# Kernel tuning notes

Measured on AMD Instinct MI355X. Metric: run time of the kernel, lower is better.

## Reference

```python
import jax, jax.numpy as jnp
import numpy as np

DIM = 512
HEADS = 8
DK = DIM // HEADS
MAX_LEN = 22118
EPS = 1e-5


def _layernorm(h, g, b):
    m = jnp.mean(h, axis=-1, keepdims=True)
    v = jnp.mean((h - m) ** 2, axis=-1, keepdims=True)
    return (h - m) / jnp.sqrt(v + EPS) * g + b


def setup_inputs() -> dict:
    key = jax.random.key(0)
    ks = jax.random.split(key, 16)
    B, S = 4, 2048
    xavier = lambda k, shp: jax.random.normal(k, shp, jnp.float32) * np.sqrt(2.0 / (shp[0] + shp[1]))
    return {
        "x": jax.random.normal(ks[0], (B, S, DIM), jnp.float32),
        "vis_data": jax.random.normal(ks[1], (B, S, DIM), jnp.float32),
        "coord1": jax.random.randint(ks[2], (B, S), 0, MAX_LEN, jnp.int32),
        "coord2": jax.random.randint(ks[3], (B, S), 0, MAX_LEN, jnp.int32),
        "emb1": jax.random.normal(ks[4], (MAX_LEN, DIM // 2), jnp.float32) * 0.02,
        "emb2": jax.random.normal(ks[5], (MAX_LEN, DIM // 2), jnp.float32) * 0.02,
        "wq": xavier(ks[6], (DIM, DIM)), "bq": jnp.zeros((DIM,), jnp.float32),
        "wk": xavier(ks[7], (DIM, DIM)), "bk": jnp.zeros((DIM,), jnp.float32),
        "wv": xavier(ks[8], (DIM, DIM)), "bv": jnp.zeros((DIM,), jnp.float32),
        "w1": xavier(ks[9], (DIM, DIM)), "b1": jnp.zeros((DIM,), jnp.float32),
        "g1": jnp.ones((DIM,), jnp.float32), "beta1": jnp.zeros((DIM,), jnp.float32),
        "w2": xavier(ks[10], (DIM, DIM)), "b2": jnp.zeros((DIM,), jnp.float32),
        "g2": jnp.ones((DIM,), jnp.float32), "beta2": jnp.zeros((DIM,), jnp.float32),
    }


def reference(x, vis_data, coord1, coord2, emb1, emb2, wq, bq, wk, bk, wv, bv,
              w1, b1, g1, beta1, w2, b2, g2, beta2):
    B, S, _ = x.shape
    # learned positional encoding: concat of two coordinate embeddings
    pos = jnp.concatenate([emb1[coord1], emb2[coord2]], axis=-1)  # [B,S,DIM]
    xp = x + pos
    # Q/K from vis_data, V from position-encoded x
    q = (vis_data @ wq + bq).reshape(B, S, HEADS, DK)
    k = (vis_data @ wk + bk).reshape(B, S, HEADS, DK)
    v = (xp @ wv + bv).reshape(B, S, HEADS, DK)
    scores = jnp.einsum("bqhd,bkhd->bhqk", q, k) / np.sqrt(DK).astype(np.float32)
    attn = jax.nn.softmax(scores, axis=-1)  # dropout is identity in eval
    out = jnp.einsum("bhqk,bkhd->bqhd", attn, v).reshape(B, S, DIM)
    # post-attention MLP stack (self.layer)
    h = jax.nn.leaky_relu(out @ w1 + b1, negative_slope=0.2)
    h = _layernorm(h, g1, beta1)
    h = jax.nn.leaky_relu(h @ w2 + b2, negative_slope=0.2)
    h = _layernorm(h, g2, beta2)
    return h
```

## Files before the change

### kernel.cpp

```cpp
#include <hip/hip_runtime.h>

#define DIM 512
#define SEQ 2048
#define MROWS 8192

typedef short short8 __attribute__((ext_vector_type(8)));
typedef float floatx4 __attribute__((ext_vector_type(4)));

__device__ __forceinline__ ushort f2bf(float f) {
  union { float f; unsigned u; } v; v.f = f;
  unsigned r = v.u + 0x7fff + ((v.u >> 16) & 1);
  return (ushort)(r >> 16);
}
__device__ __forceinline__ float bf2f(ushort u) {
  union { unsigned u; float f; } v; v.u = ((unsigned)u) << 16;
  return v.f;
}

__global__ __launch_bounds__(256) void prep_wtrans_kernel(
    const float* __restrict__ x, const float* __restrict__ vis,
    const int* __restrict__ c1, const int* __restrict__ c2,
    const float* __restrict__ e1, const float* __restrict__ e2,
    const float* __restrict__ wq, const float* __restrict__ wk,
    const float* __restrict__ wv, const float* __restrict__ w1,
    const float* __restrict__ w2,
    ushort* __restrict__ xp_bf, ushort* __restrict__ vis_bf,
    ushort* __restrict__ wt_qkv, ushort* __restrict__ wt1,
    ushort* __restrict__ wt2) {
  __shared__ float Ls[64 * 65];
  if (blockIdx.x < 4096) {
    int gid = blockIdx.x * 256 + threadIdx.x;
    int row = gid >> 7;
    int col = (gid & 127) * 4;
    float4 vv = *(const float4*)(vis + (size_t)row * 512 + col);
    ushort4 vb; vb.x = f2bf(vv.x); vb.y = f2bf(vv.y); vb.z = f2bf(vv.z); vb.w = f2bf(vv.w);
    *(ushort4*)(vis_bf + (size_t)row * 512 + col) = vb;
    float4 p;
    if (col < 256) p = *(const float4*)(e1 + (size_t)c1[row] * 256 + col);
    else           p = *(const float4*)(e2 + (size_t)c2[row] * 256 + col - 256);
    float4 xv = *(const float4*)(x + (size_t)row * 512 + col);
    ushort4 xb; xb.x = f2bf(xv.x + p.x); xb.y = f2bf(xv.y + p.y);
    xb.z = f2bf(xv.z + p.z); xb.w = f2bf(xv.w + p.w);
    *(ushort4*)(xp_bf + (size_t)row * 512 + col) = xb;
  } else {
    int bid = blockIdx.x - 4096;
    int mid = bid >> 6;
    int tile = bid & 63;
    int k0 = (tile >> 3) * 64, n0 = (tile & 7) * 64;
    const float* W = mid == 0 ? wq : mid == 1 ? wk : mid == 2 ? wv : mid == 3 ? w1 : w2;
    ushort* outp = mid < 3 ? (wt_qkv + (size_t)mid * 512 * 512) : (mid == 3 ? wt1 : wt2);
    float scale = (mid == 0) ? 0.125f : 1.0f;
    int r = threadIdx.x >> 4, c4 = (threadIdx.x & 15) * 4;
#pragma unroll
    for (int i = 0; i < 4; i++) {
      int row = i * 16 + r;
      float4 wv4 = *(const float4*)(W + (size_t)(k0 + row) * 512 + n0 + c4);
      Ls[row * 65 + c4 + 0] = wv4.x * scale;
      Ls[row * 65 + c4 + 1] = wv4.y * scale;
      Ls[row * 65 + c4 + 2] = wv4.z * scale;
      Ls[row * 65 + c4 + 3] = wv4.w * scale;
    }
    __syncthreads();
    int n = threadIdx.x >> 2, kc = (threadIdx.x & 3) * 16;
    ushort pk[16];
#pragma unroll
    for (int i = 0; i < 16; i++) pk[i] = f2bf(Ls[(kc + i) * 65 + n]);
    ushort* op = outp + (size_t)(n0 + n) * 512 + k0 + kc;
    *(uint4*)op = *(uint4*)pk;
    *(uint4*)(op + 8) = *(uint4*)(pk + 8);
  }
}

template <bool LEAKY>
__global__ __launch_bounds__(256, 4) void gemm_mfma(
    const ushort* __restrict__ A01, const ushort* __restrict__ A2,
    const ushort* __restrict__ Wt,
    const float* __restrict__ bias0, const float* __restrict__ bias1,
    const float* __restrict__ bias2,
    ushort* __restrict__ out0, ushort* __restrict__ out1,
    ushort* __restrict__ out2, float s0scale) {
  __shared__ __align__(16) ushort Sm[12288];
  ushort* As = Sm;
  ushort* Bs = Sm + 4096;
  int t = threadIdx.x;
  int seg = blockIdx.x >> 2;
  int nloc0 = (blockIdx.x & 3) * 128;
  int n0w = blockIdx.x * 128;
  int m0 = blockIdx.y * 64;
  const ushort* A = (seg < 2) ? A01 : A2;
  const float* bias = seg == 0 ? bias0 : seg == 1 ? bias1 : bias2;
  ushort* out = seg == 0 ? out0 : seg == 1 ? out1 : out2;
  float bscale = seg == 0 ? s0scale : 1.0f;

  int w = t >> 6, lane = t & 63;
  int wm = (w & 1) * 32, wn = (w >> 1) * 64;
  int quad = lane >> 4, lcol = lane & 15;
  int arow = t >> 2, ach = (t & 3) * 2;
  int brow = t >> 1, bch = (t & 1) * 4;

  floatx4 acc[2][4] = {};

  for (int k0 = 0; k0 < 512; k0 += 64) {
    __syncthreads();
#pragma unroll
    for (int i = 0; i < 2; i++) {
      int ch = ach + i;
      *(uint4*)(&As[arow * 64 + (ch ^ (arow & 7)) * 8]) =
          *(const uint4*)(A + (size_t)(m0 + arow) * 512 + k0 + ch * 8);
    }
#pragma unroll
    for (int j = 0; j < 4; j++) {
      int ch = bch + j;
      *(uint4*)(&Bs[brow * 64 + (ch ^ (brow & 7)) * 8]) =
          *(const uint4*)(Wt + (size_t)(n0w + brow) * 512 + k0 + ch * 8);
    }
    __syncthreads();
#pragma unroll
    for (int kc = 0; kc < 2; kc++) {
      int pch = ((kc * 4 + quad) ^ (lcol & 7)) * 8;
      short8 af[2], bfr[4];
#pragma unroll
      for (int i = 0; i < 2; i++)
        af[i] = *(const short8*)(&As[(wm + i * 16 + lcol) * 64 + pch]);
#pragma unroll
      for (int i = 0; i < 4; i++)
        bfr[i] = *(const short8*)(&Bs[(wn + i * 16 + lcol) * 64 + pch]);
#pragma unroll
      for (int mt = 0; mt < 2; mt++)
#pragma unroll
        for (int nt = 0; nt < 4; nt++)
          acc[mt][nt] = __builtin_amdgcn_mfma_f32_16x16x32_bf16(
              af[mt], bfr[nt], acc[mt][nt], 0, 0, 0);
    }
  }

  __syncthreads();
  float* Ls = (float*)Sm + w * 1088;
  int rr = lane >> 2, cc = (lane & 3) * 16;
#pragma unroll
  for (int mt = 0; mt < 2; mt++) {
#pragma unroll
    for (int nt = 0; nt < 4; nt++) {
      float bv = bias[nloc0 + wn + nt * 16 + lcol] * bscale;
#pragma unroll
      for (int r = 0; r < 4; r++) {
        float vv = acc[mt][nt][r] + bv;
        if (LEAKY) vv = vv >= 0.f ? vv : 0.2f * vv;
        Ls[(quad * 4 + r) * 68 + nt * 16 + lcol] = vv;
      }
    }
    asm volatile("s_waitcnt lgkmcnt(0)" ::: "memory");
    ushort pk[16];
#pragma unroll
    for (int i = 0; i < 16; i += 4) {
      float4 fv = *(const float4*)(&Ls[rr * 68 + cc + i]);
      pk[i] = f2bf(fv.x); pk[i + 1] = f2bf(fv.y);
      pk[i + 2] = f2bf(fv.z); pk[i + 3] = f2bf(fv.w);
    }
    ushort* op = out + (size_t)(m0 + wm + mt * 16 + rr) * 512 + nloc0 + wn + cc;
    *(uint4*)op = *(uint4*)pk;
    *(uint4*)(op + 8) = *(uint4*)(pk + 8);
    asm volatile("s_waitcnt lgkmcnt(0)" ::: "memory");
  }
}

__global__ __launch_bounds__(256, 2) void attn_mfma_kernel(
    const ushort* __restrict__ q, const ushort* __restrict__ k,
    const ushort* __restrict__ v, ushort* __restrict__ out) {
  __shared__ __align__(16) ushort Ks[128 * 64];
  __shared__ __align__(16) ushort Vt[64 * 128];
  __shared__ __align__(16) ushort Ps[4 * 32 * 64];
  int t = threadIdx.x;
  int blk = blockIdx.x;
  int qt = blk & 15, h = (blk >> 4) & 7, b = blk >> 7;
  int wave = t >> 6, lane = t & 63, quad = lane >> 4, lcol = lane & 15;
  int q0 = qt * 128 + wave * 32;
  const size_t base = (size_t)b * SEQ * 512 + h * 64;

  short8 qf[2][2];
#pragma unroll
  for (int qm = 0; qm < 2; qm++)
#pragma unroll
    for (int kc = 0; kc < 2; kc++)
      qf[qm][kc] = *(const short8*)(
          q + base + (size_t)(q0 + qm * 16 + lcol) * 512 + kc * 32 + quad * 8);

  floatx4 O[2][4] = {};
  float lsum[2][4] = {};

  ushort* Pw = Ps + wave * (32 * 64);
  int krow = t >> 1, khalf = t & 1;
  int pl = t & 63, dg = t >> 6;

  for (int kt = 0; kt < SEQ; kt += 128) {
    __syncthreads();
#pragma unroll
    for (int j = 0; j < 4; j++) {
      int ch = khalf * 4 + j;
      *(uint4*)(&Ks[krow * 64 + (ch ^ (krow & 7)) * 8]) =
          *(const uint4*)(k + base + (size_t)(kt + krow) * 512 + ch * 8);
    }
    {
      uint4 va[2], vb[2];
      const ushort* vr0 = v + base + (size_t)(kt + 2 * pl) * 512 + dg * 16;
      const ushort* vr1 = vr0 + 512;
      va[0] = *(const uint4*)(vr0); va[1] = *(const uint4*)(vr0 + 8);
      vb[0] = *(const uint4*)(vr1); vb[1] = *(const uint4*)(vr1 + 8);
      const ushort* a0 = (const ushort*)va;
      const ushort* a1 = (const ushort*)vb;
#pragma unroll
      for (int i = 0; i < 16; i++) {
        int dim = dg * 16 + i;
        unsigned pack = (unsigned)a0[i] | ((unsigned)a1[i] << 16);
        int pch = (pl >> 2) ^ (dim & 7);
        *(unsigned*)(&Vt[dim * 128 + pch * 8 + (pl & 3) * 2]) = pack;
      }
    }
    __syncthreads();

#pragma unroll
    for (int half = 0; half < 2; half++) {
#pragma unroll
      for (int qm = 0; qm < 2; qm++) {
        floatx4 S[4] = {};
#pragma unroll
        for (int kc = 0; kc < 2; kc++) {
          int pch = ((kc * 4 + quad) ^ (lcol & 7)) * 8;
#pragma unroll
          for (int jt4 = 0; jt4 < 4; jt4++) {
            int jrow = (half * 4 + jt4) * 16 + lcol;
            short8 kf = *(const short8*)(&Ks[jrow * 64 + pch]);
            S[jt4] = __builtin_amdgcn_mfma_f32_16x16x32_bf16(
                qf[qm][kc], kf, S[jt4], 0, 0, 0);
          }
        }
#pragma unroll
        for (int jt4 = 0; jt4 < 4; jt4++)
#pragma unroll
          for (int r = 0; r < 4; r++) {
            float p = __expf(S[jt4][r]);
            lsum[qm][r] += p;
            int prow = qm * 16 + quad * 4 + r;
            int pcol = jt4 * 16 + lcol;
            int pch2 = (pcol >> 3) ^ (prow & 7);
            Pw[prow * 64 + pch2 * 8 + (pcol & 7)] =
                (ushort)(__float_as_uint(p) >> 16);
          }
      }
      asm volatile("s_waitcnt lgkmcnt(0)" ::: "memory");
#pragma unroll
      for (int qm = 0; qm < 2; qm++) {
#pragma unroll
        for (int kc = 0; kc < 2; kc++) {
          short8 pf = *(const short8*)(
              &Pw[(qm * 16 + lcol) * 64 + ((kc * 4 + quad) ^ (lcol & 7)) * 8]);
#pragma unroll
          for (int nt = 0; nt < 4; nt++) {
            int dim = nt * 16 + lcol;
            int ch = half * 8 + kc * 4 + quad;
            short8 vf = *(const short8*)(&Vt[dim * 128 + (ch ^ (lcol & 7)) * 8]);
            O[qm][nt] = __builtin_amdgcn_mfma_f32_16x16x32_bf16(
                pf, vf, O[qm][nt], 0, 0, 0);
          }
        }
      }
    }
  }

#pragma unroll
  for (int qm = 0; qm < 2; qm++)
#pragma unroll
    for (int r = 0; r < 4; r++) {
#pragma unroll
      for (int m = 1; m <= 8; m <<= 1)
        lsum[qm][r] += __shfl_xor(lsum[qm][r], m, 64);
      lsum[qm][r] = 1.f / lsum[qm][r];
    }
#pragma unroll
  for (int qm = 0; qm < 2; qm++)
#pragma unroll
    for (int nt = 0; nt < 4; nt++)
#pragma unroll
      for (int r = 0; r < 4; r++)
        out[base + (size_t)(q0 + qm * 16 + quad * 4 + r) * 512 + nt * 16 + lcol] =
            f2bf(O[qm][nt][r] * lsum[qm][r]);
}

template <bool OUTF32>
__global__ __launch_bounds__(256) void ln_kernel(
    const ushort* __restrict__ h, const float* __restrict__ g,
    const float* __restrict__ beta, void* __restrict__ outv) {
  int wave = threadIdx.x >> 6, lane = threadIdx.x & 63;
  int row = blockIdx.x * 4 + wave;
  uint4 raw = *(const uint4*)(h + (size_t)row * 512 + lane * 8);
  const ushort* hu = (const ushort*)&raw;
  float vals[8];
#pragma unroll
  for (int i = 0; i < 8; i++) vals[i] = bf2f(hu[i]);
  float sum = 0.f;
#pragma unroll
  for (int i = 0; i < 8; i++) sum += vals[i];
#pragma unroll
  for (int off = 32; off >= 1; off >>= 1) sum += __shfl_xor(sum, off, 64);
  float mean = sum * (1.f / 512.f);
  float vs = 0.f;
#pragma unroll
  for (int i = 0; i < 8; i++) { float d = vals[i] - mean; vs += d * d; }
#pragma unroll
  for (int off = 32; off >= 1; off >>= 1) vs += __shfl_xor(vs, off, 64);
  float rstd = rsqrtf(vs * (1.f / 512.f) + 1e-5f);
  float4 gv0 = *(const float4*)(g + lane * 8);
  float4 gv1 = *(const float4*)(g + lane * 8 + 4);
  float4 bv0 = *(const float4*)(beta + lane * 8);
  float4 bv1 = *(const float4*)(beta + lane * 8 + 4);
  float gr[8] = {gv0.x, gv0.y, gv0.z, gv0.w, gv1.x, gv1.y, gv1.z, gv1.w};
  float br[8] = {bv0.x, bv0.y, bv0.z, bv0.w, bv1.x, bv1.y, bv1.z, bv1.w};
  float res[8];
#pragma unroll
  for (int i = 0; i < 8; i++) res[i] = (vals[i] - mean) * rstd * gr[i] + br[i];
  if (OUTF32) {
    float* op = (float*)outv + (size_t)row * 512 + lane * 8;
    float4 o0, o1;
    o0.x = res[0]; o0.y = res[1]; o0.z = res[2]; o0.w = res[3];
    o1.x = res[4]; o1.y = res[5]; o1.z = res[6]; o1.w = res[7];
    *(float4*)op = o0; *(float4*)(op + 4) = o1;
  } else {
    ushort* op = (ushort*)outv + (size_t)row * 512 + lane * 8;
    ushort4 o0, o1;
    o0.x = f2bf(res[0]); o0.y = f2bf(res[1]); o0.z = f2bf(res[2]); o0.w = f2bf(res[3]);
    o1.x = f2bf(res[4]); o1.y = f2bf(res[5]); o1.z = f2bf(res[6]); o1.w = f2bf(res[7]);
    *(ushort4*)op = o0; *(ushort4*)(op + 4) = o1;
  }
}

extern "C" void kernel_launch(void* const* d_in, const int* in_sizes, int n_in,
                              void* d_out, int out_size, void* d_ws,
                              size_t ws_size, hipStream_t stream) {
  (void)in_sizes; (void)n_in; (void)out_size; (void)ws_size;
  const float* x     = (const float*)d_in[0];
  const float* vis   = (const float*)d_in[1];
  const int*   c1    = (const int*)d_in[2];
  const int*   c2    = (const int*)d_in[3];
  const float* e1    = (const float*)d_in[4];
  const float* e2    = (const float*)d_in[5];
  const float* wq    = (const float*)d_in[6];
  const float* bq    = (const float*)d_in[7];
  const float* wk    = (const float*)d_in[8];
  const float* bk    = (const float*)d_in[9];
  const float* wv    = (const float*)d_in[10];
  const float* bv    = (const float*)d_in[11];
  const float* w1    = (const float*)d_in[12];
  const float* b1    = (const float*)d_in[13];
  const float* g1    = (const float*)d_in[14];
  const float* beta1 = (const float*)d_in[15];
  const float* w2    = (const float*)d_in[16];
  const float* b2    = (const float*)d_in[17];
  const float* g2    = (const float*)d_in[18];
  const float* beta2 = (const float*)d_in[19];
  float* out = (float*)d_out;
  ushort* ws = (ushort*)d_ws;

  const size_t BUF = (size_t)MROWS * 512;
  ushort* xp_bf  = ws;
  ushort* vis_bf = ws + BUF;
  ushort* q_bf   = ws + 2 * BUF;
  ushort* k_bf   = ws + 3 * BUF;
  ushort* v_bf   = ws + 4 * BUF;
  ushort* wt_qkv = ws + 5 * BUF;
  ushort* wt1    = wt_qkv + 1536 * 512;
  ushort* wt2    = wt1 + 512 * 512;
  ushort* attn_bf = vis_bf;
  ushort* h1_bf   = xp_bf;
  ushort* ln1_bf  = q_bf;
  ushort* h2_bf   = k_bf;

  prep_wtrans_kernel<<<4416, 256, 0, stream>>>(
      x, vis, c1, c2, e1, e2, wq, wk, wv, w1, w2, xp_bf, vis_bf, wt_qkv, wt1, wt2);
  gemm_mfma<false><<<dim3(12, 128), 256, 0, stream>>>(
      vis_bf, xp_bf, wt_qkv, bq, bk, bv, q_bf, k_bf, v_bf, 0.125f);
  attn_mfma_kernel<<<512, 256, 0, stream>>>(q_bf, k_bf, v_bf, attn_bf);
  gemm_mfma<true><<<dim3(4, 128), 256, 0, stream>>>(
      attn_bf, attn_bf, wt1, b1, b1, b1, h1_bf, h1_bf, h1_bf, 1.0f);
  ln_kernel<false><<<2048, 256, 0, stream>>>(h1_bf, g1, beta1, ln1_bf);
  gemm_mfma<true><<<dim3(4, 128), 256, 0, stream>>>(
      ln1_bf, ln1_bf, wt2, b2, b2, b2, h2_bf, h2_bf, h2_bf, 1.0f);
  ln_kernel<true><<<2048, 256, 0, stream>>>(h2_bf, g2, beta2, out);
}
```

Measured before the change: 269.2 us.

## Double-buffer K/V tiles with async LDS loads in attention kernel

The attention kernel now keeps two LDS buffers for K and transposed V. The next K tile is fetched with global_load_lds and the next V tile is prefetched into registers while the current tile is computed, leaving one barrier per iteration. The MFMA operands are swapped so the score accumulators come out transposed, which lets P be packed with v_cvt_pk_bf16_f32 and written in wider stores, cuts the row-sum reduction to two shuffles, and vectorizes the output stores. It also adds s_setprio around MFMA bursts and remaps block indices so blocks sharing a batch/head are spread. The cost is doubled LDS for K/V, which may reduce occupancy, plus added register pressure.

```diff
diff --git a/kernel.cpp b/kernel.cpp
--- a/kernel.cpp
+++ b/kernel.cpp
@@ -167,11 +167,12 @@
 __global__ __launch_bounds__(256, 2) void attn_mfma_kernel(
     const ushort* __restrict__ q, const ushort* __restrict__ k,
     const ushort* __restrict__ v, ushort* __restrict__ out) {
-  __shared__ __align__(16) ushort Ks[128 * 64];
-  __shared__ __align__(16) ushort Vt[64 * 128];
-  __shared__ __align__(16) ushort Ps[4 * 32 * 64];
+  __shared__ __align__(16) ushort Ks[2][128 * 64];
+  __shared__ __align__(16) ushort Vt[2][64 * 128];
+  __shared__ __align__(16) unsigned Pp[4096];
   int t = threadIdx.x;
   int blk = blockIdx.x;
+  blk = ((blk & 7) << 6) | (blk >> 3);
   int qt = blk & 15, h = (blk >> 4) & 7, b = blk >> 7;
   int wave = t >> 6, lane = t & 63, quad = lane >> 4, lcol = lane & 15;
   int q0 = qt * 128 + wave * 32;
@@ -186,104 +187,155 @@
           q + base + (size_t)(q0 + qm * 16 + lcol) * 512 + kc * 32 + quad * 8);
 
   floatx4 O[2][4] = {};
-  float lsum[2][4] = {};
-
-  ushort* Pw = Ps + wave * (32 * 64);
-  int krow = t >> 1, khalf = t & 1;
+  float lsum[2] = {0.f, 0.f};
+
+  unsigned* Ppw = Pp + wave * 1024;
   int pl = t & 63, dg = t >> 6;
-
-  for (int kt = 0; kt < SEQ; kt += 128) {
-    __syncthreads();
-#pragma unroll
-    for (int j = 0; j < 4; j++) {
-      int ch = khalf * 4 + j;
-      *(uint4*)(&Ks[krow * 64 + (ch ^ (krow & 7)) * 8]) =
-          *(const uint4*)(k + base + (size_t)(kt + krow) * 512 + ch * 8);
-    }
-    {
-      uint4 va[2], vb[2];
-      const ushort* vr0 = v + base + (size_t)(kt + 2 * pl) * 512 + dg * 16;
-      const ushort* vr1 = vr0 + 512;
-      va[0] = *(const uint4*)(vr0); va[1] = *(const uint4*)(vr0 + 8);
-      vb[0] = *(const uint4*)(vr1); vb[1] = *(const uint4*)(vr1 + 8);
+  int l8 = lane >> 3, l7 = lane & 7;
+  int kchs = (l7 ^ l8) * 8;
+  const ushort* vbase = v + base + (size_t)(2 * pl) * 512 + dg * 16;
+
+  uint4 va[2], vb[2];
+
+#pragma unroll
+  for (int j = 0; j < 4; j++) {
+    const ushort* gp = k + base + (size_t)((wave * 4 + j) * 8 + l8) * 512 + kchs;
+    __builtin_amdgcn_global_load_lds(
+        (const __attribute__((address_space(1))) unsigned*)gp,
+        (__attribute__((address_space(3))) unsigned*)(&Ks[0][(wave * 4 + j) * 512]),
+        16, 0, 0);
+  }
+  va[0] = *(const uint4*)(vbase);       va[1] = *(const uint4*)(vbase + 8);
+  vb[0] = *(const uint4*)(vbase + 512); vb[1] = *(const uint4*)(vbase + 520);
+  {
+    const ushort* a0 = (const ushort*)va;
+    const ushort* a1 = (const ushort*)vb;
+#pragma unroll
+    for (int i = 0; i < 16; i++) {
+      int dim = dg * 16 + i;
+      unsigned pack = (unsigned)a0[i] | ((unsigned)a1[i] << 16);
+      int pch = (pl >> 2) ^ (dim & 7);
+      *(unsigned*)(&Vt[0][dim * 128 + pch * 8 + (pl & 3) * 2]) = pack;
+    }
+  }
+  __syncthreads();
+
+  int cb = 0;
+  for (int it = 0; it < 16; it++) {
+    if (it < 15) {
+      int ktn = (it + 1) * 128;
+#pragma unroll
+      for (int j = 0; j < 4; j++) {
+        const ushort* gp =
+            k + base + (size_t)(ktn + (wave * 4 + j) * 8 + l8) * 512 + kchs;
+        __builtin_amdgcn_global_load_lds(
+            (const __attribute__((address_space(1))) unsigned*)gp,
+            (__attribute__((address_space(3))) unsigned*)(
+                &Ks[cb ^ 1][(wave * 4 + j) * 512]),
+            16, 0, 0);
+      }
+      const ushort* vr = vbase + (size_t)ktn * 512;
+      va[0] = *(const uint4*)(vr);       va[1] = *(const uint4*)(vr + 8);
+      vb[0] = *(const uint4*)(vr + 512); vb[1] = *(const uint4*)(vr + 520);
+    }
+
+    const ushort* Ksb = Ks[cb];
+    const ushort* Vtb = Vt[cb];
+#pragma unroll
+    for (int half = 0; half < 2; half++) {
+      short8 kf[2][4];
+#pragma unroll
+      for (int kc = 0; kc < 2; kc++) {
+        int pch = ((kc * 4 + quad) ^ (lcol & 7)) * 8;
+#pragma unroll
+        for (int jt = 0; jt < 4; jt++)
+          kf[kc][jt] =
+              *(const short8*)(&Ksb[((half * 4 + jt) * 16 + lcol) * 64 + pch]);
+      }
+#pragma unroll
+      for (int qm = 0; qm < 2; qm++) {
+        floatx4 S[4] = {};
+        __builtin_amdgcn_s_setprio(1);
+#pragma unroll
+        for (int kc = 0; kc < 2; kc++)
+#pragma unroll
+          for (int jt = 0; jt < 4; jt++)
+            S[jt] = __builtin_amdgcn_mfma_f32_16x16x32_bf16(
+                kf[kc][jt], qf[qm][kc], S[jt], 0, 0, 0);
+        __builtin_amdgcn_s_setprio(0);
+#pragma unroll
+        for (int jt = 0; jt < 4; jt++) {
+          float e0 = __expf(S[jt][0]);
+          float e1 = __expf(S[jt][1]);
+          float e2 = __expf(S[jt][2]);
+          float e3 = __expf(S[jt][3]);
+          lsum[qm] += (e0 + e1) + (e2 + e3);
+          unsigned p0, p1;
+          asm("v_cvt_pk_bf16_f32 %0, %1, %2" : "=v"(p0) : "v"(e0), "v"(e1));
+          asm("v_cvt_pk_bf16_f32 %0, %1, %2" : "=v"(p1) : "v"(e2), "v"(e3));
+          int c0 = 2 * jt + (quad >> 1);
+          uint2 pk2; pk2.x = p0; pk2.y = p1;
+          *(uint2*)(Ppw + qm * 512 + lcol * 32 + ((c0 ^ (lcol & 7)) << 2) +
+                    (quad & 1) * 2) = pk2;
+        }
+      }
+      asm volatile("s_waitcnt lgkmcnt(0)" ::: "memory");
+#pragma unroll
+      for (int kc = 0; kc < 2; kc++) {
+        short8 vf[4];
+        int ch = half * 8 + kc * 4 + quad;
+#pragma unroll
+        for (int nt = 0; nt < 4; nt++)
+          vf[nt] = *(const short8*)(
+              &Vtb[(nt * 16 + lcol) * 128 + ((ch ^ (lcol & 7)) * 8)]);
+#pragma unroll
+        for (int qm = 0; qm < 2; qm++) {
+          short8 pf = *(const short8*)(Ppw + qm * 512 + lcol * 32 +
+                                       (((kc * 4 + quad) ^ (lcol & 7)) << 2));
+          __builtin_amdgcn_s_setprio(1);
+#pragma unroll
+          for (int nt = 0; nt < 4; nt++)
+            O[qm][nt] = __builtin_amdgcn_mfma_f32_16x16x32_bf16(
+                vf[nt], pf, O[qm][nt], 0, 0, 0);
+          __builtin_amdgcn_s_setprio(0);
+        }
+      }
+    }
+
+    if (it < 15) {
       const ushort* a0 = (const ushort*)va;
       const ushort* a1 = (const ushort*)vb;
+      ushort* Vtn = Vt[cb ^ 1];
 #pragma unroll
       for (int i = 0; i < 16; i++) {
         int dim = dg * 16 + i;
         unsigned pack = (unsigned)a0[i] | ((unsigned)a1[i] << 16);
         int pch = (pl >> 2) ^ (dim & 7);
-        *(unsigned*)(&Vt[dim * 128 + pch * 8 + (pl & 3) * 2]) = pack;
-      }
-    }
+        *(unsigned*)(&Vtn[dim * 128 + pch * 8 + (pl & 3) * 2]) = pack;
+      }
+    }
+    asm volatile("s_waitcnt vmcnt(0)" ::: "memory");
     __syncthreads();
-
-#pragma unroll
-    for (int half = 0; half < 2; half++) {
-#pragma unroll
-      for (int qm = 0; qm < 2; qm++) {
-        floatx4 S[4] = {};
-#pragma unroll
-        for (int kc = 0; kc < 2; kc++) {
-          int pch = ((kc * 4 + quad) ^ (lcol & 7)) * 8;
-#pragma unroll
-          for (int jt4 = 0; jt4 < 4; jt4++) {
-            int jrow = (half * 4 + jt4) * 16 + lcol;
-            short8 kf = *(const short8*)(&Ks[jrow * 64 + pch]);
-            S[jt4] = __builtin_amdgcn_mfma_f32_16x16x32_bf16(
-                qf[qm][kc], kf, S[jt4], 0, 0, 0);
-          }
-        }
-#pragma unroll
-        for (int jt4 = 0; jt4 < 4; jt4++)
-#pragma unroll
-          for (int r = 0; r < 4; r++) {
-            float p = __expf(S[jt4][r]);
-            lsum[qm][r] += p;
-            int prow = qm * 16 + quad * 4 + r;
-            int pcol = jt4 * 16 + lcol;
-            int pch2 = (pcol >> 3) ^ (prow & 7);
-            Pw[prow * 64 + pch2 * 8 + (pcol & 7)] =
-                (ushort)(__float_as_uint(p) >> 16);
-          }
-      }
-      asm volatile("s_waitcnt lgkmcnt(0)" ::: "memory");
-#pragma unroll
-      for (int qm = 0; qm < 2; qm++) {
-#pragma unroll
-        for (int kc = 0; kc < 2; kc++) {
-          short8 pf = *(const short8*)(
-              &Pw[(qm * 16 + lcol) * 64 + ((kc * 4 + quad) ^ (lcol & 7)) * 8]);
-#pragma unroll
-          for (int nt = 0; nt < 4; nt++) {
-            int dim = nt * 16 + lcol;
-            int ch = half * 8 + kc * 4 + quad;
-            short8 vf = *(const short8*)(&Vt[dim * 128 + (ch ^ (lcol & 7)) * 8]);
-            O[qm][nt] = __builtin_amdgcn_mfma_f32_16x16x32_bf16(
-                pf, vf, O[qm][nt], 0, 0, 0);
-          }
-        }
-      }
-    }
-  }
-
-#pragma unroll
-  for (int qm = 0; qm < 2; qm++)
-#pragma unroll
-    for (int r = 0; r < 4; r++) {
-#pragma unroll
-      for (int m = 1; m <= 8; m <<= 1)
-        lsum[qm][r] += __shfl_xor(lsum[qm][r], m, 64);
-      lsum[qm][r] = 1.f / lsum[qm][r];
-    }
-#pragma unroll
-  for (int qm = 0; qm < 2; qm++)
-#pragma unroll
-    for (int nt = 0; nt < 4; nt++)
-#pragma unroll
-      for (int r = 0; r < 4; r++)
-        out[base + (size_t)(q0 + qm * 16 + quad * 4 + r) * 512 + nt * 16 + lcol] =
-            f2bf(O[qm][nt][r] * lsum[qm][r]);
+    cb ^= 1;
+  }
+
+#pragma unroll
+  for (int qm = 0; qm < 2; qm++) {
+    float s = lsum[qm];
+    s += __shfl_xor(s, 16, 64);
+    s += __shfl_xor(s, 32, 64);
+    float rl = 1.f / s;
+#pragma unroll
+    for (int nt = 0; nt < 4; nt++) {
+      ushort4 o;
+      o.x = f2bf(O[qm][nt][0] * rl);
+      o.y = f2bf(O[qm][nt][1] * rl);
+      o.z = f2bf(O[qm][nt][2] * rl);
+      o.w = f2bf(O[qm][nt][3] * rl);
+      *(ushort4*)(out + base + (size_t)(q0 + qm * 16 + lcol) * 512 +
+                  nt * 16 + quad * 4) = o;
+    }
+  }
 }
 
 template <bool OUTF32>
```

Result: faster. 262.0 us (-2.7%).
